# Optimization experiments

Hardware: AMD Instinct MI355X
Metric: run time of the kernel (lower is better)

## Reference

```python
import jax, jax.numpy as jnp
import numpy as np

K = 3          # conv kernel size
PW = 4         # parallel window (pw_height == pw_width)
OC = 128       # out_channels
IC = 128       # in_channels
RANK = 256
STRIDE = PW - K + 1  # 2


def _sdk_weight_map(kernel):
    # kernel: [O, C, K, K] numpy. Concat all (top,left) zero-pad placements into PWxPW.
    O, C, k, _ = kernel.shape
    d = PW - k
    maps = []
    for top in range(d + 1):
        for left in range(d + 1):
            pk = np.zeros((O, C, PW, PW), dtype=kernel.dtype)
            pk[:, :, top:top + k, left:left + k] = kernel
            maps.append(pk.reshape(O, -1))
    return np.concatenate(maps, axis=0)  # [(d+1)^2 * O, C*PW*PW]


def setup_inputs() -> dict:
    rng = np.random.default_rng(0)
    kernel = (rng.standard_normal((OC, IC, K, K)) * 0.05).astype(np.float32)
    W = _sdk_weight_map(kernel)  # [512, 2048]
    u, s, vh = np.linalg.svd(W, full_matrices=False)
    Q = (u[:, :RANK] * s[:RANK]).astype(np.float32)   # u_t @ diag(s_t)
    R = vh[:RANK].astype(np.float32)
    key = jax.random.key(0)
    x = jax.random.normal(key, (32, 128, 64, 64), dtype=jnp.float32)
    return {"x": x, "Q": jnp.asarray(Q), "R": jnp.asarray(R)}


def _slice_and_forward(x, Q, R):
    N, C, H, Wd = x.shape
    s = STRIDE
    pad_v = (H + 2 - PW) % s
    pad_h = (Wd + 2 - PW) % s
    ov = -(-(H + 2 - PW) // s) + 1   # ceil div + 1 (matches math.ceil(...)+1)
    oh = -(-(Wd + 2 - PW) // s) + 1
    xp = jnp.pad(x, ((0, 0), (0, 0), (1, 1 + pad_v), (1, 1 + pad_h)))
    # im2col / unfold: feature layout C slowest, then (i, j) within window -> matches F.unfold
    wins = [xp[:, :, i:i + s * (ov - 1) + 1:s, j:j + s * (oh - 1) + 1:s]
            for i in range(PW) for j in range(PW)]
    patches = jnp.stack(wins, axis=2)                      # [N, C, PW*PW, ov, oh]
    flat = patches.reshape(N, C * PW * PW, ov * oh).transpose(0, 2, 1)  # [N, L, C*PW*PW]
    # F.linear(flat, Q @ R) == (flat @ R^T) @ Q^T  (apply low-rank factors sequentially)
    lin = jnp.einsum('nlr,mr->nlm', jnp.einsum('nlf,rf->nlr', flat, R), Q)  # [N, L, s*s*OC]
    lin = lin.reshape(N, ov, oh, s, s, OC).transpose(0, 1, 3, 2, 4, 5)
    lin = lin.reshape(N, H + pad_v // 2, Wd + pad_h // 2, OC)
    lin = lin.transpose(0, 3, 1, 2)                        # NHWC -> NCHW
    return lin[:, :, :H, :Wd]


def reference(x, Q, R):
    return _slice_and_forward(x, Q, R)
```

## Files before the change

kernel.cpp:

```cpp
#include <hip/hip_runtime.h>
#include <hip/hip_bf16.h>

typedef __attribute__((ext_vector_type(8))) short short8;
typedef __attribute__((ext_vector_type(4))) float f32x4;
typedef unsigned int uint;
typedef __attribute__((ext_vector_type(4))) uint uint4v;

#define AS1 __attribute__((address_space(1)))
#define AS3 __attribute__((address_space(3)))

#define QB_OFF  (1u << 20)
#define XPH_OFF (1310720u)

__device__ __forceinline__ uint bf16r(float f) {
    uint u = __float_as_uint(f);
    u += 0x7FFFu + ((u >> 16) & 1u);
    return u >> 16;
}
__device__ __forceinline__ uint pk2(float lo, float hi) {
    return bf16r(lo) | (bf16r(hi) << 16);
}

__global__ __launch_bounds__(256) void prep_kernel(
    const float* __restrict__ x, const float* __restrict__ Q, const float* __restrict__ R,
    char* __restrict__ Rp4, char* __restrict__ Qp4, char* __restrict__ xph)
{
    const int bid = blockIdx.x, tid = threadIdx.x;
    if (bid < 2048) {
        __shared__ float xt[128 * 65];
        const int n = bid >> 6, h = bid & 63;
        {
            const int c = tid >> 1, half = tid & 1;
            const float4* src = (const float4*)(x + (((size_t)(n * 128 + c) * 64 + h) * 64 + half * 32));
            #pragma unroll
            for (int q = 0; q < 8; ++q) {
                float4 v = src[q];
                float* d = &xt[c * 65 + half * 32 + q * 4];
                d[0] = v.x; d[1] = v.y; d[2] = v.z; d[3] = v.w;
            }
        }
        __syncthreads();
        {
            const int w = tid >> 2, cq = tid & 3;
            uint pw[16];
            #pragma unroll
            for (int m = 0; m < 16; ++m)
                pw[m] = pk2(xt[(cq * 32 + 2 * m) * 65 + w], xt[(cq * 32 + 2 * m + 1) * 65 + w]);
            char* dst = xph + (size_t)n * 1115136 + (size_t)(h + 1) * 16896 + (w + 1) * 256 + cq * 64;
            #pragma unroll
            for (int i = 0; i < 4; ++i) {
                uint4v q4 = { pw[4 * i], pw[4 * i + 1], pw[4 * i + 2], pw[4 * i + 3] };
                *(uint4v*)(dst + i * 16) = q4;
            }
        }
        if (tid < 32) {
            int side = tid >> 4, e = tid & 15;
            uint4v z = {0, 0, 0, 0};
            *(uint4v*)(xph + (size_t)n * 1115136 + (size_t)(h + 1) * 16896 + side * 65 * 256 + e * 16) = z;
        }
        if (h == 0) {
            uint4v z = {0, 0, 0, 0};
            #pragma unroll
            for (int it = 0; it < 9; ++it) {
                int idx = tid + it * 256;
                if (idx < 2112) {
                    int rr = (idx >= 1056) ? 65 : 0;
                    int jj = idx - (rr ? 1056 : 0);
                    int col = jj >> 4, e = jj & 15;
                    *(uint4v*)(xph + (size_t)n * 1115136 + (size_t)rr * 16896 + col * 256 + e * 16) = z;
                }
            }
        }
    } else if (bid < 2304) {
        int g = (bid - 2048) * 256 + tid;
        int s = g >> 10, p = g & 1023;
        int col = p >> 2, wu = p & 3;
        const float* src = R + (size_t)col * 2048 + (((s & 3) * 32 + wu * 8) * 16 + (s >> 2));
        uint pw[4];
        #pragma unroll
        for (int m = 0; m < 4; ++m)
            pw[m] = pk2(src[(2 * m) * 16], src[(2 * m + 1) * 16]);
        uint4v q4 = { pw[0], pw[1], pw[2], pw[3] };
        *(uint4v*)(Rp4 + (size_t)s * 16384 + p * 16) = q4;
    } else {
        int g = (bid - 2304) * 256 + tid;
        int ks = g >> 11, p = g & 2047;
        int col = p >> 2, unit = p & 3;
        const float4* s = (const float4*)(Q + (size_t)col * 256 + ks * 32 + unit * 8);
        float4 a = s[0], b = s[1];
        uint4v q4 = { pk2(a.x, a.y), pk2(a.z, a.w), pk2(b.x, b.y), pk2(b.z, b.w) };
        *(uint4v*)(Qp4 + (size_t)ks * 32768 + p * 16) = q4;
    }
}

__global__ __launch_bounds__(512, 2) void fused_kernel(
    const char* __restrict__ xph, const char* __restrict__ Rp4,
    const char* __restrict__ Qp4, float* __restrict__ out)
{
    extern __shared__ __align__(16) char lds[];

    const int blk = blockIdx.x;
    const int b = (blk & 7) * 32 + (blk >> 3);
    const int n = b >> 3, vt = b & 7;
    const int tid = threadIdx.x;
    const int wave = tid >> 6, lane = tid & 63;
    const int lr = lane & 15, kg = lane >> 4;
    const int lr7 = lr & 7;
    const int wm = wave >> 2, wn = wave & 3;

    const char* xbase = xph + (size_t)n * 1115136;
    const int u16 = tid * 16;

    const int xm = tid >> 2, xcu = tid & 3;
    const int xc = (8 * vt + 2 * (xm >> 5)) * 16896 + (2 * (xm & 31)) * 256 + xcu * 16;

    const int a0 = wm * 4096 + lr * 64 + kg * 16;
    const int bb0 = wn * 4096 + lr * 64 + kg * 16;

    int tb[4];
    #pragma unroll
    for (int mf = 0; mf < 4; ++mf) tb[mf] = (wm * 64 + mf * 16 + lr) * 512;
    const int tswz = (lr7 << 4) ^ ((lr & 8) << 2);
    int qbase[8];
    #pragma unroll
    for (int nf = 0; nf < 8; ++nf)
        qbase[nf] = ((wn >> 1) * 256 + (nf >> 2) * 128 + (wn & 1) * 64 + (nf & 3) * 16 + lr) * 64 + kg * 16;

#define BDMA2(s_) { _Pragma("unroll") for (int q = 0; q < 2; ++q)                       \
        __builtin_amdgcn_global_load_lds(                                               \
            (const AS1 void*)(Rp4 + (size_t)(s_) * 16384 + q * 8192 + u16),             \
            (AS3 void*)(lds + 32768 + ((s_) & 3) * 16384 + q * 8192 + u16), 16, 0, 0); }
#define XDMA1(s_) __builtin_amdgcn_global_load_lds(                                     \
        (const AS1 void*)(xbase + xc + ((s_) >> 4) * 16896 + (((s_) >> 2) & 3) * 256 + ((s_) & 3) * 64), \
        (AS3 void*)(lds + ((s_) & 3) * 8192 + u16), 16, 0, 0);
#define QDMA(ks_) { _Pragma("unroll") for (int q = 0; q < 4; ++q)                       \
        __builtin_amdgcn_global_load_lds(                                               \
            (const AS1 void*)(Qp4 + (size_t)(ks_) * 32768 + q * 8192 + u16),            \
            (AS3 void*)(lds + (((ks_) & 1) ? 65536 : 98304) + q * 8192 + u16), 16, 0, 0); }

#define BAR(Nstr) { __builtin_amdgcn_sched_barrier(0);                                  \
        asm volatile("s_waitcnt vmcnt(" Nstr ") lgkmcnt(0)\n\ts_barrier" ::: "memory"); \
        __builtin_amdgcn_sched_barrier(0); }
#define LBAR { __builtin_amdgcn_sched_barrier(0);                                       \
        asm volatile("s_waitcnt lgkmcnt(0)\n\ts_barrier" ::: "memory");                 \
        __builtin_amdgcn_sched_barrier(0); }

    f32x4 acc[4][4];
    #pragma unroll
    for (int i = 0; i < 4; ++i)
        #pragma unroll
        for (int j = 0; j < 4; ++j) acc[i][j] = (f32x4)0.f;

    BDMA2(0) XDMA1(0) BDMA2(1) XDMA1(1) BDMA2(2) XDMA1(2)
    BAR("6")

    #pragma unroll
    for (int s = 0; s < 64; ++s) {
        if (s <= 60) { BDMA2(s + 3) XDMA1(s + 3) }
        if (s == 60) QDMA(0)
        const char* xs = lds + (s & 3) * 8192;
        const char* bs = lds + 32768 + (s & 3) * 16384;
        short8 af[4], bf[4];
        #pragma unroll
        for (int mf = 0; mf < 4; ++mf)
            af[mf] = *(const short8*)(xs + a0 + mf * 1024);
        #pragma unroll
        for (int nf = 0; nf < 4; ++nf)
            bf[nf] = *(const short8*)(bs + bb0 + nf * 1024);
        #pragma unroll
        for (int nf = 0; nf < 4; ++nf)
            #pragma unroll
            for (int mf = 0; mf < 4; ++mf)
                acc[mf][nf] = __builtin_amdgcn_mfma_f32_16x16x32_bf16(af[mf], bf[nf], acc[mf][nf], 0, 0, 0);
        if (s <= 59)      { BAR("6") }
        else if (s == 60) { BAR("10") }
        else if (s == 61) { BAR("7") }
        else              { BAR("4") }
    }

    QDMA(1)
    #pragma unroll
    for (int mf = 0; mf < 4; ++mf)
        #pragma unroll
        for (int nf = 0; nf < 4; ++nf)
            #pragma unroll
            for (int r = 0; r < 4; ++r) {
                int row = wm * 64 + mf * 16 + kg * 4 + r;
                int col = wn * 64 + nf * 16 + lr;
                *(ushort*)(lds + row * 512 +
                           ((col * 2) ^ ((row & 7) << 4) ^ ((row & 8) << 2))) =
                    (ushort)bf16r(acc[mf][nf][r]);
            }
    BAR("4")

    f32x4 acc2[4][8];
    #pragma unroll
    for (int i = 0; i < 4; ++i)
        #pragma unroll
        for (int j = 0; j < 8; ++j) acc2[i][j] = (f32x4)0.f;
    #pragma unroll
    for (int ks = 0; ks < 8; ++ks) {
        if (ks >= 1 && ks <= 6) QDMA(ks + 1)
        const char* qs = lds + ((ks & 1) ? 65536 : 98304);
        short8 af2[4];
        #pragma unroll
        for (int mf = 0; mf < 4; ++mf)
            af2[mf] = *(const short8*)(lds + tb[mf] + ((ks * 64 + kg * 16) ^ tswz));
        #pragma unroll
        for (int nf = 0; nf < 8; ++nf) {
            const short8 bq = *(const short8*)(qs + qbase[nf]);
            #pragma unroll
            for (int mf = 0; mf < 4; ++mf)
                acc2[mf][nf] = __builtin_amdgcn_mfma_f32_16x16x32_bf16(af2[mf], bq, acc2[mf][nf], 0, 0, 0);
        }
        if (ks <= 6) { BAR("0") }
    }

    const int si = wn >> 1, ochalf = wn & 1;
    #pragma unroll
    for (int mh = 0; mh < 4; ++mh) {
        LBAR
        if (wm == (mh >> 1)) {
            #pragma unroll
            for (int mfh = 0; mfh < 2; ++mfh) {
                const int mf = (mh & 1) * 2 + mfh;
                #pragma unroll
                for (int q = 0; q < 4; ++q) {
                    const int oc = ochalf * 64 + q * 16 + lr;
                    const int ub = si * 34816 + oc * 272 + (((4 * mfh + kg) ^ (oc & 7)) << 5);
                    f32x4 v0 = { acc2[mf][q][0], acc2[mf][4 + q][0], acc2[mf][q][1], acc2[mf][4 + q][1] };
                    f32x4 v1 = { acc2[mf][q][2], acc2[mf][4 + q][2], acc2[mf][q][3], acc2[mf][4 + q][3] };
                    *(f32x4*)(lds + ub) = v0;
                    *(f32x4*)(lds + ub + 16) = v1;
                }
            }
        }
        LBAR
        #pragma unroll
        for (int it = 0; it < 8; ++it) {
            int uidx = it * 512 + tid;
            int w4 = uidx & 15, oc = (uidx >> 4) & 127, sie = uidx >> 11;
            f32x4 v = *(const f32x4*)(lds + sie * 34816 + oc * 272 + ((w4 ^ (2 * (oc & 7))) << 4));
            *(f32x4*)(out + (size_t)n * 524288 + (size_t)oc * 4096
                          + (8 * vt + 2 * mh + sie) * 64 + w4 * 4) = v;
        }
    }
}

extern "C" void kernel_launch(void* const* d_in, const int* in_sizes, int n_in,
                              void* d_out, int out_size, void* d_ws, size_t ws_size,
                              hipStream_t stream) {
    const float* x = (const float*)d_in[0];
    const float* Q = (const float*)d_in[1];
    const float* R = (const float*)d_in[2];
    float* out = (float*)d_out;

    char* ws = (char*)d_ws;
    char* Rp4 = ws;
    char* Qp4 = ws + QB_OFF;
    char* xph = ws + XPH_OFF;

    prep_kernel<<<2368, 256, 0, stream>>>(x, Q, R, Rp4, Qp4, xph);
    fused_kernel<<<256, 512, 131072, stream>>>(xph, Rp4, Qp4, out);
}
```

Baseline: 80.60 us.

## Halve fused GEMM tile per block, double grid, read Q directly from global

The fused kernel now uses 256-thread blocks covering 64 rows instead of 512 threads covering 128 rows, launching 512 blocks with 64KB of LDS each, so more blocks can be resident and the grid is finer. The R/x staging drops from a 4-deep to a 3-deep ring, and the R packing layout in prep is rearranged to match. The second GEMM reads Q fragments straight from global memory instead of staging them through LDS with barriers, and the MFMA section is wrapped in s_setprio. The cost is more global traffic for R and Q, since each half-size block reloads the full weight stream, and a shallower prefetch pipeline.

```diff
diff --git a/kernel.cpp b/kernel.cpp
--- a/kernel.cpp
+++ b/kernel.cpp
@@ -73,70 +73,64 @@
         }
     } else if (bid < 2304) {
         int g = (bid - 2048) * 256 + tid;
-        int s = g >> 10, p = g & 1023;
-        int col = p >> 2, wu = p & 3;
-        const float* src = R + (size_t)col * 2048 + (((s & 3) * 32 + wu * 8) * 16 + (s >> 2));
+        int s = g >> 10, rem = g & 1023;
+        int cu = rem >> 8, col = rem & 255;
+        const float* src = R + (size_t)col * 2048 + (((s & 3) * 32 + cu * 8) * 16 + (s >> 2));
         uint pw[4];
         #pragma unroll
         for (int m = 0; m < 4; ++m)
             pw[m] = pk2(src[(2 * m) * 16], src[(2 * m + 1) * 16]);
         uint4v q4 = { pw[0], pw[1], pw[2], pw[3] };
-        *(uint4v*)(Rp4 + (size_t)s * 16384 + p * 16) = q4;
+        *(uint4v*)(Rp4 + (size_t)g * 16) = q4;
     } else {
         int g = (bid - 2304) * 256 + tid;
         int ks = g >> 11, p = g & 2047;
-        int col = p >> 2, unit = p & 3;
-        const float4* s = (const float4*)(Q + (size_t)col * 256 + ks * 32 + unit * 8);
+        int col = p >> 2, cu = p & 3;
+        const float4* s = (const float4*)(Q + (size_t)col * 256 + ks * 32 + cu * 8);
         float4 a = s[0], b = s[1];
         uint4v q4 = { pk2(a.x, a.y), pk2(a.z, a.w), pk2(b.x, b.y), pk2(b.z, b.w) };
         *(uint4v*)(Qp4 + (size_t)ks * 32768 + p * 16) = q4;
     }
 }
 
-__global__ __launch_bounds__(512, 2) void fused_kernel(
+__global__ __launch_bounds__(256, 2) void fused_kernel(
     const char* __restrict__ xph, const char* __restrict__ Rp4,
     const char* __restrict__ Qp4, float* __restrict__ out)
 {
     extern __shared__ __align__(16) char lds[];
 
     const int blk = blockIdx.x;
-    const int b = (blk & 7) * 32 + (blk >> 3);
-    const int n = b >> 3, vt = b & 7;
+    const int b = (blk & 7) * 64 + (blk >> 3);
+    const int n = b >> 4, vt = b & 15;
     const int tid = threadIdx.x;
     const int wave = tid >> 6, lane = tid & 63;
     const int lr = lane & 15, kg = lane >> 4;
     const int lr7 = lr & 7;
-    const int wm = wave >> 2, wn = wave & 3;
+    const int wn = wave;
 
     const char* xbase = xph + (size_t)n * 1115136;
     const int u16 = tid * 16;
 
-    const int xm = tid >> 2, xcu = tid & 3;
-    const int xc = (8 * vt + 2 * (xm >> 5)) * 16896 + (2 * (xm & 31)) * 256 + xcu * 16;
-
-    const int a0 = wm * 4096 + lr * 64 + kg * 16;
-    const int bb0 = wn * 4096 + lr * 64 + kg * 16;
-
-    int tb[4];
-    #pragma unroll
-    for (int mf = 0; mf < 4; ++mf) tb[mf] = (wm * 64 + mf * 16 + lr) * 512;
-    const int tswz = (lr7 << 4) ^ ((lr & 8) << 2);
-    int qbase[8];
+    const int xrh = lane >> 5, xcl = lane & 31;
+    const int xc0 = (4 * vt + 2 * xrh) * 16896 + (2 * xcl) * 256 + wave * 16;
+
+    const int a0  = kg * 1024 + lr * 16;
+    const int bb0 = kg * 4096 + wn * 1024 + lr * 16;
+
+    const int t0 = (wn * 8 + (lr >> 3)) * 1024 + (lr & 7) * 2;
+
+    int qoff[8];
     #pragma unroll
     for (int nf = 0; nf < 8; ++nf)
-        qbase[nf] = ((wn >> 1) * 256 + (nf >> 2) * 128 + (wn & 1) * 64 + (nf & 3) * 16 + lr) * 64 + kg * 16;
-
-#define BDMA2(s_) { _Pragma("unroll") for (int q = 0; q < 2; ++q)                       \
+        qoff[nf] = ((wn >> 1) * 256 + (nf >> 2) * 128 + (wn & 1) * 64 + (nf & 3) * 16 + lr) * 64 + kg * 16;
+
+#define BDMA(s_) { _Pragma("unroll") for (int q = 0; q < 4; ++q)                        \
         __builtin_amdgcn_global_load_lds(                                               \
-            (const AS1 void*)(Rp4 + (size_t)(s_) * 16384 + q * 8192 + u16),             \
-            (AS3 void*)(lds + 32768 + ((s_) & 3) * 16384 + q * 8192 + u16), 16, 0, 0); }
-#define XDMA1(s_) __builtin_amdgcn_global_load_lds(                                     \
-        (const AS1 void*)(xbase + xc + ((s_) >> 4) * 16896 + (((s_) >> 2) & 3) * 256 + ((s_) & 3) * 64), \
-        (AS3 void*)(lds + ((s_) & 3) * 8192 + u16), 16, 0, 0);
-#define QDMA(ks_) { _Pragma("unroll") for (int q = 0; q < 4; ++q)                       \
-        __builtin_amdgcn_global_load_lds(                                               \
-            (const AS1 void*)(Qp4 + (size_t)(ks_) * 32768 + q * 8192 + u16),            \
-            (AS3 void*)(lds + (((ks_) & 1) ? 65536 : 98304) + q * 8192 + u16), 16, 0, 0); }
+            (const AS1 void*)(Rp4 + (size_t)(s_) * 16384 + q * 4096 + u16),             \
+            (AS3 void*)(lds + 12288 + ((s_) % 3) * 16384 + q * 4096 + u16), 16, 0, 0); }
+#define XDMA(s_) __builtin_amdgcn_global_load_lds(                                      \
+        (const AS1 void*)(xbase + xc0 + ((s_) >> 4) * 16896 + (((s_) >> 2) & 3) * 256 + ((s_) & 3) * 64), \
+        (AS3 void*)(lds + ((s_) % 3) * 4096 + u16), 16, 0, 0);
 
 #define BAR(Nstr) { __builtin_amdgcn_sched_barrier(0);                                  \
         asm volatile("s_waitcnt vmcnt(" Nstr ") lgkmcnt(0)\n\ts_barrier" ::: "memory"); \
@@ -151,47 +145,41 @@
         #pragma unroll
         for (int j = 0; j < 4; ++j) acc[i][j] = (f32x4)0.f;
 
-    BDMA2(0) XDMA1(0) BDMA2(1) XDMA1(1) BDMA2(2) XDMA1(2)
-    BAR("6")
+    BDMA(0) XDMA(0) BDMA(1) XDMA(1)
+    BAR("5")
 
     #pragma unroll
     for (int s = 0; s < 64; ++s) {
-        if (s <= 60) { BDMA2(s + 3) XDMA1(s + 3) }
-        if (s == 60) QDMA(0)
-        const char* xs = lds + (s & 3) * 8192;
-        const char* bs = lds + 32768 + (s & 3) * 16384;
+        if (s <= 61) { BDMA(s + 2) XDMA(s + 2) }
+        const char* xs = lds + (s % 3) * 4096;
+        const char* bs = lds + 12288 + (s % 3) * 16384;
         short8 af[4], bf[4];
         #pragma unroll
         for (int mf = 0; mf < 4; ++mf)
-            af[mf] = *(const short8*)(xs + a0 + mf * 1024);
+            af[mf] = *(const short8*)(xs + a0 + mf * 256);
         #pragma unroll
         for (int nf = 0; nf < 4; ++nf)
-            bf[nf] = *(const short8*)(bs + bb0 + nf * 1024);
+            bf[nf] = *(const short8*)(bs + bb0 + nf * 256);
+        __builtin_amdgcn_s_setprio(1);
         #pragma unroll
         for (int nf = 0; nf < 4; ++nf)
             #pragma unroll
             for (int mf = 0; mf < 4; ++mf)
                 acc[mf][nf] = __builtin_amdgcn_mfma_f32_16x16x32_bf16(af[mf], bf[nf], acc[mf][nf], 0, 0, 0);
-        if (s <= 59)      { BAR("6") }
-        else if (s == 60) { BAR("10") }
-        else if (s == 61) { BAR("7") }
-        else              { BAR("4") }
-    }
-
-    QDMA(1)
+        __builtin_amdgcn_s_setprio(0);
+        if (s <= 61) { BAR("5") } else { BAR("0") }
+    }
+
     #pragma unroll
     for (int mf = 0; mf < 4; ++mf)
         #pragma unroll
         for (int nf = 0; nf < 4; ++nf)
             #pragma unroll
             for (int r = 0; r < 4; ++r) {
-                int row = wm * 64 + mf * 16 + kg * 4 + r;
-                int col = wn * 64 + nf * 16 + lr;
-                *(ushort*)(lds + row * 512 +
-                           ((col * 2) ^ ((row & 7) << 4) ^ ((row & 8) << 2))) =
+                *(ushort*)(lds + t0 + nf * 2048 + (mf * 16 + kg * 4 + r) * 16) =
                     (ushort)bf16r(acc[mf][nf][r]);
             }
-    BAR("4")
+    LBAR
 
     f32x4 acc2[4][8];
     #pragma unroll
@@ -200,49 +188,44 @@
         for (int j = 0; j < 8; ++j) acc2[i][j] = (f32x4)0.f;
     #pragma unroll
     for (int ks = 0; ks < 8; ++ks) {
-        if (ks >= 1 && ks <= 6) QDMA(ks + 1)
-        const char* qs = lds + ((ks & 1) ? 65536 : 98304);
         short8 af2[4];
         #pragma unroll
         for (int mf = 0; mf < 4; ++mf)
-            af2[mf] = *(const short8*)(lds + tb[mf] + ((ks * 64 + kg * 16) ^ tswz));
+            af2[mf] = *(const short8*)(lds + ks * 4096 + a0 + mf * 256);
         #pragma unroll
         for (int nf = 0; nf < 8; ++nf) {
-            const short8 bq = *(const short8*)(qs + qbase[nf]);
+            const short8 bq = *(const short8*)(Qp4 + (size_t)ks * 32768 + qoff[nf]);
             #pragma unroll
             for (int mf = 0; mf < 4; ++mf)
                 acc2[mf][nf] = __builtin_amdgcn_mfma_f32_16x16x32_bf16(af2[mf], bq, acc2[mf][nf], 0, 0, 0);
         }
-        if (ks <= 6) { BAR("0") }
     }
 
     const int si = wn >> 1, ochalf = wn & 1;
     #pragma unroll
-    for (int mh = 0; mh < 4; ++mh) {
+    for (int p = 0; p < 2; ++p) {
         LBAR
-        if (wm == (mh >> 1)) {
-            #pragma unroll
-            for (int mfh = 0; mfh < 2; ++mfh) {
-                const int mf = (mh & 1) * 2 + mfh;
-                #pragma unroll
-                for (int q = 0; q < 4; ++q) {
-                    const int oc = ochalf * 64 + q * 16 + lr;
-                    const int ub = si * 34816 + oc * 272 + (((4 * mfh + kg) ^ (oc & 7)) << 5);
-                    f32x4 v0 = { acc2[mf][q][0], acc2[mf][4 + q][0], acc2[mf][q][1], acc2[mf][4 + q][1] };
-                    f32x4 v1 = { acc2[mf][q][2], acc2[mf][4 + q][2], acc2[mf][q][3], acc2[mf][4 + q][3] };
-                    *(f32x4*)(lds + ub) = v0;
-                    *(f32x4*)(lds + ub + 16) = v1;
-                }
+        #pragma unroll
+        for (int mfh = 0; mfh < 2; ++mfh) {
+            const int mf = 2 * p + mfh;
+            #pragma unroll
+            for (int q = 0; q < 4; ++q) {
+                const int oc = ochalf * 64 + q * 16 + lr;
+                const int ub = si * 32768 + oc * 256 + (((4 * mfh + kg) ^ lr7) << 5);
+                f32x4 v0 = { acc2[mf][q][0], acc2[mf][4 + q][0], acc2[mf][q][1], acc2[mf][4 + q][1] };
+                f32x4 v1 = { acc2[mf][q][2], acc2[mf][4 + q][2], acc2[mf][q][3], acc2[mf][4 + q][3] };
+                *(f32x4*)(lds + ub) = v0;
+                *(f32x4*)(lds + ub + 16) = v1;
             }
         }
         LBAR
         #pragma unroll
-        for (int it = 0; it < 8; ++it) {
-            int uidx = it * 512 + tid;
+        for (int it = 0; it < 16; ++it) {
+            int uidx = it * 256 + tid;
             int w4 = uidx & 15, oc = (uidx >> 4) & 127, sie = uidx >> 11;
-            f32x4 v = *(const f32x4*)(lds + sie * 34816 + oc * 272 + ((w4 ^ (2 * (oc & 7))) << 4));
+            f32x4 v = *(const f32x4*)(lds + sie * 32768 + oc * 256 + ((w4 ^ (2 * (oc & 7))) << 4));
             *(f32x4*)(out + (size_t)n * 524288 + (size_t)oc * 4096
-                          + (8 * vt + 2 * mh + sie) * 64 + w4 * 4) = v;
+                          + (vt * 4 + p * 2 + sie) * 64 + w4 * 4) = v;
         }
     }
 }
@@ -261,5 +244,5 @@
     char* xph = ws + XPH_OFF;
 
     prep_kernel<<<2368, 256, 0, stream>>>(x, Q, R, Rp4, Qp4, xph);
-    fused_kernel<<<256, 512, 131072, stream>>>(xph, Rp4, Qp4, out);
-}
+    fused_kernel<<<512, 256, 65536, stream>>>(xph, Rp4, Qp4, out);
+}
```

New measurement: 89.42 us. +10.9%, slower.
